# Optimization experiments

Measured on AMD Instinct MI355X. Metric: run time of the kernel, lower is better.

## Reference

```python
import jax, jax.numpy as jnp
import numpy as np

EPS = 1e-5


def _layer_norm(x, gamma, beta):
    mu = jnp.mean(x, axis=-1, keepdims=True)
    var = jnp.var(x, axis=-1, keepdims=True)
    return (x - mu) * jax.lax.rsqrt(var + EPS) * gamma + beta


def setup_inputs() -> dict:
    key = jax.random.key(0)
    B, I, H = 4096, 1024, 1024
    ks = jax.random.split(key, 6)
    x = jax.random.normal(ks[0], (B, I), dtype=jnp.float32)
    h = jax.random.normal(ks[1], (B, H), dtype=jnp.float32)
    c = jax.random.normal(ks[2], (B, H), dtype=jnp.float32)
    # nn.Linear(I+H, 4H): weight [4H, I+H], bias [4H]
    bound = 1.0 / np.sqrt(I + H)
    W = jax.random.uniform(ks[3], (4 * H, I + H), minval=-bound, maxval=bound, dtype=jnp.float32)
    b = jax.random.uniform(ks[4], (4 * H,), minval=-bound, maxval=bound, dtype=jnp.float32)
    inp = {"x": x, "h": h, "c": c, "W": W, "b": b}
    for name in ("i", "f", "g", "o", "c"):
        inp[f"ln_{name}_g"] = jnp.ones((H,), dtype=jnp.float32)
        inp[f"ln_{name}_b"] = jnp.zeros((H,), dtype=jnp.float32)
    return inp


def reference(x, h, c, W, b, ln_i_g, ln_i_b, ln_f_g, ln_f_b, ln_g_g, ln_g_b,
              ln_o_g, ln_o_b, ln_c_g, ln_c_b):
    H = h.shape[-1]
    xh = jnp.concatenate([x, h], axis=-1)              # [B, I+H]
    gates = xh @ W.T + b                               # [B, 4H]
    i_raw, f_raw, g_raw, o_raw = jnp.split(gates, 4, axis=-1)
    i = jax.nn.sigmoid(_layer_norm(i_raw, ln_i_g, ln_i_b))
    f = jax.nn.sigmoid(_layer_norm(f_raw, ln_f_g, ln_f_b))
    g = jnp.tanh(_layer_norm(g_raw, ln_g_g, ln_g_b))
    o = jax.nn.sigmoid(_layer_norm(o_raw, ln_o_g, ln_o_b))
    c_new = f * c + i * g
    h_new = o * jnp.tanh(_layer_norm(c_new, ln_c_g, ln_c_b))
    return (h_new, c_new)
```

## Files before the change

kernel.cpp:

```cpp
#include <hip/hip_runtime.h>
#include <hip/hip_bf16.h>

#define B_ROWS 4096
#define H_DIM  1024
#define K_DIM  2048
#define N_DIM  4096
#define NT     32

typedef __attribute__((ext_vector_type(8))) short bf16x8;
typedef __attribute__((ext_vector_type(4))) float f32x4;

__device__ __forceinline__ unsigned short f2bf(float f) {
  union { float f; unsigned int u; } v; v.f = f;
  unsigned int u = v.u;
  return (unsigned short)((u + 0x7fffu + ((u >> 16) & 1u)) >> 16);
}
__device__ __forceinline__ float bf2f(unsigned short u) {
  union { unsigned int u; float f; } v; v.u = ((unsigned int)u) << 16;
  return v.f;
}

__device__ __forceinline__ void gload_lds16(const void* g, void* l) {
  __builtin_amdgcn_global_load_lds(
      (const __attribute__((address_space(1))) void*)g,
      (__attribute__((address_space(3))) void*)l, 16, 0, 0);
}

__global__ __launch_bounds__(256) void pack_kernel(
    const float* __restrict__ x, const float* __restrict__ h,
    const float* __restrict__ W, unsigned short* __restrict__ Abf,
    unsigned short* __restrict__ Wbf) {
  int bid = blockIdx.x;
  if (bid < 8192) {
    int t = bid * 256 + threadIdx.x;
    int e = t * 4;
    int row = e >> 11;
    int col = e & 2047;
    const float* src = (col < 1024) ? (x + (size_t)row * 1024 + col)
                                    : (h + (size_t)row * 1024 + (col - 1024));
    float4 v = *(const float4*)src;
    ushort4 o;
    o.x = f2bf(v.x); o.y = f2bf(v.y); o.z = f2bf(v.z); o.w = f2bf(v.w);
    *(ushort4*)(Abf + e) = o;
  } else {
    int t = (bid - 8192) * 256 + threadIdx.x;
    int e = t * 4;
    float4 v = *(const float4*)(W + e);
    ushort4 o;
    o.x = f2bf(v.x); o.y = f2bf(v.y); o.z = f2bf(v.z); o.w = f2bf(v.w);
    *(ushort4*)(Wbf + e) = o;
  }
}


#define STAGE(g, kt, dst) do {                              \
    gload_lds16((g) + (size_t)(kt) * 64, (dst));            \
    gload_lds16((g) + (size_t)(kt) * 64 + 32, (dst) + 1024); } while (0)

#define WAIT_LGKM0() do {                                   \
    asm volatile("s_waitcnt lgkmcnt(0)" ::: "memory");      \
    __builtin_amdgcn_sched_barrier(0); } while (0)

#define UNR _Pragma("unroll")

#define TILE(tt, BUF, B0R, B0W)                                              \
  {                                                                          \
    char* const Lc = lds + (BUF) * 65536;                                    \
    char* const Ln = lds + ((BUF) ^ 1) * 65536;                              \
    const int kt1 = ((tt) + 1) & (NT - 1);                                   \
    const int kt2 = ((tt) + 2) & (NT - 1);                                   \
        \
    STAGE(gA1, kt1, Ln + rbA1 * 2048);                                       \
    __builtin_amdgcn_s_barrier();                                            \
    WAIT_LGKM0();                                                            \
    __builtin_amdgcn_s_setprio(1);                                           \
    UNR for (int ni = 0; ni < 2; ++ni)                                       \
      UNR for (int kk = 0; kk < 2; ++kk)                                     \
        b1[ni][kk] = *(const bf16x8*)(Lc + 32768 +                           \
            (((wn * 4 + 2 + ni) * 2 + kk) << 10) + lofs);                    \
    UNR for (int mi = 0; mi < 4; ++mi)                                       \
      UNR for (int ni = 0; ni < 2; ++ni)                                     \
        UNR for (int kk = 0; kk < 2; ++kk)                                   \
          acc[mi][ni] = __builtin_amdgcn_mfma_f32_16x16x32_bf16(             \
              a0[mi][kk], B0R[ni][kk], acc[mi][ni], 0, 0, 0);                \
    __builtin_amdgcn_s_setprio(0);                                           \
    __builtin_amdgcn_s_barrier();                                            \
         \
    STAGE(gA0, kt2, Lc + rbA0 * 2048);                                       \
    __builtin_amdgcn_s_barrier();                                            \
    WAIT_LGKM0();                                                            \
    __builtin_amdgcn_s_setprio(1);                                           \
    UNR for (int mi = 0; mi < 4; ++mi)                                       \
      UNR for (int kk = 0; kk < 2; ++kk)                                     \
        a1[mi][kk] = *(const bf16x8*)(Lc +                                   \
            (((wm * 8 + 4 + mi) * 2 + kk) << 10) + lofs);                    \
    UNR for (int mi = 0; mi < 4; ++mi)                                       \
      UNR for (int ni = 0; ni < 2; ++ni)                                     \
        UNR for (int kk = 0; kk < 2; ++kk)                                   \
          acc[mi][2 + ni] = __builtin_amdgcn_mfma_f32_16x16x32_bf16(         \
              a0[mi][kk], b1[ni][kk], acc[mi][2 + ni], 0, 0, 0);             \
    __builtin_amdgcn_s_setprio(0);                                           \
    __builtin_amdgcn_s_barrier();                                            \
                  \
    STAGE(gB0, kt2, Lc + 32768 + rbB0 * 2048);                               \
    __builtin_amdgcn_s_barrier();                                            \
    WAIT_LGKM0();                                                            \
    __builtin_amdgcn_s_setprio(1);                                           \
    UNR for (int mi = 0; mi < 4; ++mi)                                       \
      UNR for (int ni = 0; ni < 2; ++ni)                                     \
        UNR for (int kk = 0; kk < 2; ++kk)                                   \
          acc[4 + mi][2 + ni] = __builtin_amdgcn_mfma_f32_16x16x32_bf16(     \
              a1[mi][kk], b1[ni][kk], acc[4 + mi][2 + ni], 0, 0, 0);         \
    __builtin_amdgcn_s_setprio(0);                                           \
    __builtin_amdgcn_s_barrier();                                            \
          \
    STAGE(gB1, kt2, Lc + 32768 + rbB1 * 2048);                               \
    asm volatile("s_waitcnt vmcnt(6)" ::: "memory");                         \
    __builtin_amdgcn_s_barrier();                                            \
    __builtin_amdgcn_s_setprio(1);                                           \
    UNR for (int mi = 0; mi < 4; ++mi)                                       \
      UNR for (int kk = 0; kk < 2; ++kk)                                     \
        a0[mi][kk] = *(const bf16x8*)(Ln +                                   \
            (((wm * 8 + mi) * 2 + kk) << 10) + lofs);                        \
    UNR for (int ni = 0; ni < 2; ++ni)                                       \
      UNR for (int kk = 0; kk < 2; ++kk)                                     \
        B0W[ni][kk] = *(const bf16x8*)(Ln + 32768 +                          \
            (((wn * 4 + ni) * 2 + kk) << 10) + lofs);                        \
    UNR for (int mi = 0; mi < 4; ++mi)                                       \
      UNR for (int ni = 0; ni < 2; ++ni)                                     \
        UNR for (int kk = 0; kk < 2; ++kk)                                   \
          acc[4 + mi][ni] = __builtin_amdgcn_mfma_f32_16x16x32_bf16(         \
              a1[mi][kk], B0R[ni][kk], acc[4 + mi][ni], 0, 0, 0);            \
    __builtin_amdgcn_s_setprio(0);                                           \
    __builtin_amdgcn_s_barrier();                                            \
  }

__global__ __launch_bounds__(512, 2) void gemm_kernel(
    const unsigned short* __restrict__ A, const unsigned short* __restrict__ W,
    const float* __restrict__ bias, unsigned short* __restrict__ C) {
  __shared__ __align__(16) char lds[131072];

  const int tid = threadIdx.x;
  const int w = tid >> 6, l = tid & 63;
  const int wm = w >> 2, wn = w & 3;

  const int bid = blockIdx.x;
  const int xcd = bid & 7, li = bid >> 3;
  const int by = (xcd & 3) * 4 + (li >> 3);
  const int bx = ((xcd >> 2) << 3) + (li & 7);
  const int bm = by * 256, bn = bx * 256;

  const int lofs = (((l & 15) * 64) + ((l >> 4) * 16)) ^ ((l & 8) << 2);
  const int lane_r = (l >> 2) & 15;
  const int lane_c = ((l & 3) * 8) ^ (((l >> 5) & 1) * 16);

  const int rbA0 = w + (w & 4);
  const int rbA1 = rbA0 + 4;
  const int rbB0 = ((w >> 1) << 2) + (w & 1);
  const int rbB1 = rbB0 + 2;

  const unsigned short* gA0 = A + (size_t)(bm + rbA0 * 16 + lane_r) * K_DIM + lane_c;
  const unsigned short* gA1 = A + (size_t)(bm + rbA1 * 16 + lane_r) * K_DIM + lane_c;
  const unsigned short* gB0 = W + (size_t)(bn + rbB0 * 16 + lane_r) * K_DIM + lane_c;
  const unsigned short* gB1 = W + (size_t)(bn + rbB1 * 16 + lane_r) * K_DIM + lane_c;

  char* const L0 = lds;
  char* const L1 = lds + 65536;

  f32x4 acc[8][4];
#pragma unroll
  for (int i = 0; i < 8; ++i)
#pragma unroll
    for (int j = 0; j < 4; ++j) acc[i][j] = (f32x4)0.0f;

  STAGE(gA0, 0, L0 + rbA0 * 2048);
  STAGE(gA1, 0, L0 + rbA1 * 2048);
  STAGE(gB0, 0, L0 + 32768 + rbB0 * 2048);
  STAGE(gB1, 0, L0 + 32768 + rbB1 * 2048);
  STAGE(gA0, 1, L1 + rbA0 * 2048);
  STAGE(gB0, 1, L1 + 32768 + rbB0 * 2048);
  STAGE(gB1, 1, L1 + 32768 + rbB1 * 2048);
  asm volatile("s_waitcnt vmcnt(6)" ::: "memory");
  __builtin_amdgcn_s_barrier();

  bf16x8 a0[4][2], a1[4][2], b0P[2][2], b0Q[2][2], b1[2][2];

#pragma unroll
  for (int mi = 0; mi < 4; ++mi)
#pragma unroll
    for (int kk = 0; kk < 2; ++kk)
      a0[mi][kk] = *(const bf16x8*)(L0 + (((wm * 8 + mi) * 2 + kk) << 10) + lofs);
#pragma unroll
  for (int ni = 0; ni < 2; ++ni)
#pragma unroll
    for (int kk = 0; kk < 2; ++kk)
      b0P[ni][kk] = *(const bf16x8*)(L0 + 32768 + (((wn * 4 + ni) * 2 + kk) << 10) + lofs);

  for (int t = 0; t < NT; t += 2) {
    TILE(t, 0, b0P, b0Q);
    TILE(t + 1, 1, b0Q, b0P);
  }

  const int lm = l & 15, lq = l >> 4;
  float bv[4];
#pragma unroll
  for (int ni = 0; ni < 4; ++ni) bv[ni] = bias[bn + wn * 64 + ni * 16 + lm];
  unsigned short* Cb = C + (size_t)(bm + wm * 128) * N_DIM + bn + wn * 64;
#pragma unroll
  for (int mi = 0; mi < 8; ++mi)
#pragma unroll
    for (int j = 0; j < 4; ++j) {
      const size_t rofs = (size_t)(mi * 16 + lq * 4 + j) * N_DIM;
#pragma unroll
      for (int ni = 0; ni < 4; ++ni)
        Cb[rofs + ni * 16 + lm] = f2bf(acc[mi][ni][j] + bv[ni]);
    }
}

__device__ __forceinline__ float2 blk_sum2(float s, float q, float* red,
                                           int wid, int lane) {
#pragma unroll
  for (int o = 32; o >= 1; o >>= 1) {
    s += __shfl_xor(s, o, 64);
    q += __shfl_xor(q, o, 64);
  }
  __syncthreads();
  if (lane == 0) { red[wid * 2] = s; red[wid * 2 + 1] = q; }
  __syncthreads();
  s = red[0] + red[2] + red[4] + red[6];
  q = red[1] + red[3] + red[5] + red[7];
  return make_float2(s, q);
}

__device__ __forceinline__ float sigmoidf_(float x) {
  return 1.0f / (1.0f + __expf(-x));
}
__device__ __forceinline__ float tanhf_(float x) {
  return 1.0f - 2.0f / (__expf(2.0f * x) + 1.0f);
}

__global__ __launch_bounds__(256) void ln_lstm_kernel(
    const unsigned short* __restrict__ gates, const float* __restrict__ cprev,
    const float* __restrict__ g_i, const float* __restrict__ b_i,
    const float* __restrict__ g_f, const float* __restrict__ b_f,
    const float* __restrict__ g_g, const float* __restrict__ b_g,
    const float* __restrict__ g_o, const float* __restrict__ b_o,
    const float* __restrict__ g_c, const float* __restrict__ b_c,
    float* __restrict__ out) {
  const int b = blockIdx.x;
  const int t = threadIdx.x;
  const int wid = t >> 6, lane = t & 63;
  __shared__ float red[8];

  const unsigned short* grow = gates + (size_t)b * N_DIM;
  const int c0 = t * 4;

  float v[4][4];
#pragma unroll
  for (int g = 0; g < 4; g++) {
    ushort4 raw = *(const ushort4*)(grow + g * 1024 + c0);
    v[g][0] = bf2f(raw.x); v[g][1] = bf2f(raw.y);
    v[g][2] = bf2f(raw.z); v[g][3] = bf2f(raw.w);
  }

  const float4 gamma[4] = {*(const float4*)(g_i + c0), *(const float4*)(g_f + c0),
                           *(const float4*)(g_g + c0), *(const float4*)(g_o + c0)};
  const float4 beta[4]  = {*(const float4*)(b_i + c0), *(const float4*)(b_f + c0),
                           *(const float4*)(b_g + c0), *(const float4*)(b_o + c0)};

  float a[4][4];
#pragma unroll
  for (int g = 0; g < 4; g++) {
    float s = v[g][0] + v[g][1] + v[g][2] + v[g][3];
    float q = v[g][0]*v[g][0] + v[g][1]*v[g][1] + v[g][2]*v[g][2] + v[g][3]*v[g][3];
    float2 r = blk_sum2(s, q, red, wid, lane);
    float mu = r.x * (1.0f / 1024.0f);
    float var = r.y * (1.0f / 1024.0f) - mu * mu;
    float inv = rsqrtf(var + 1e-5f);
    const float* gm = (const float*)&gamma[g];
    const float* bt = (const float*)&beta[g];
#pragma unroll
    for (int j = 0; j < 4; j++) {
      float n = (v[g][j] - mu) * inv * gm[j] + bt[j];
      a[g][j] = (g == 2) ? tanhf_(n) : sigmoidf_(n);
    }
  }

  float4 cp = *(const float4*)(cprev + (size_t)b * 1024 + c0);
  const float* cpe = (const float*)&cp;
  float cn[4];
#pragma unroll
  for (int j = 0; j < 4; j++)
    cn[j] = a[1][j] * cpe[j] + a[0][j] * a[2][j];

  {
    float s = cn[0] + cn[1] + cn[2] + cn[3];
    float q = cn[0]*cn[0] + cn[1]*cn[1] + cn[2]*cn[2] + cn[3]*cn[3];
    float2 r = blk_sum2(s, q, red, wid, lane);
    float mu = r.x * (1.0f / 1024.0f);
    float var = r.y * (1.0f / 1024.0f) - mu * mu;
    float inv = rsqrtf(var + 1e-5f);
    float4 gm = *(const float4*)(g_c + c0);
    float4 bt = *(const float4*)(b_c + c0);
    const float* gme = (const float*)&gm;
    const float* bte = (const float*)&bt;
    float hn[4];
#pragma unroll
    for (int j = 0; j < 4; j++) {
      float n = (cn[j] - mu) * inv * gme[j] + bte[j];
      hn[j] = a[3][j] * tanhf_(n);
    }
    *(float4*)(out + (size_t)b * 1024 + c0) = make_float4(hn[0], hn[1], hn[2], hn[3]);
    *(float4*)(out + (size_t)B_ROWS * H_DIM + (size_t)b * 1024 + c0) =
        make_float4(cn[0], cn[1], cn[2], cn[3]);
  }
}

extern "C" void kernel_launch(void* const* d_in, const int* in_sizes, int n_in,
                              void* d_out, int out_size, void* d_ws,
                              size_t ws_size, hipStream_t stream) {
  const float* x    = (const float*)d_in[0];
  const float* h    = (const float*)d_in[1];
  const float* c    = (const float*)d_in[2];
  const float* W    = (const float*)d_in[3];
  const float* bias = (const float*)d_in[4];
  const float* ln_i_g = (const float*)d_in[5];
  const float* ln_i_b = (const float*)d_in[6];
  const float* ln_f_g = (const float*)d_in[7];
  const float* ln_f_b = (const float*)d_in[8];
  const float* ln_g_g = (const float*)d_in[9];
  const float* ln_g_b = (const float*)d_in[10];
  const float* ln_o_g = (const float*)d_in[11];
  const float* ln_o_b = (const float*)d_in[12];
  const float* ln_c_g = (const float*)d_in[13];
  const float* ln_c_b = (const float*)d_in[14];

  unsigned short* Abf = (unsigned short*)d_ws;
  unsigned short* Wbf = Abf + (size_t)B_ROWS * K_DIM;
  unsigned short* gates = Wbf + (size_t)N_DIM * K_DIM;

  pack_kernel<<<16384, 256, 0, stream>>>(x, h, W, Abf, Wbf);

  dim3 ggrid(256);
  gemm_kernel<<<ggrid, 512, 0, stream>>>(Abf, Wbf, bias, gates);

  ln_lstm_kernel<<<B_ROWS, 256, 0, stream>>>(
      gates, c, ln_i_g, ln_i_b, ln_f_g, ln_f_b, ln_g_g, ln_g_b,
      ln_o_g, ln_o_b, ln_c_g, ln_c_b, (float*)d_out);
}
```

Baseline: 102.3 us.

## Restructure GEMM main loop into four-stage K=32 pipeline with one barrier per tile

Replaces the two-buffer K=64 tile schedule, which had four barrier-separated MFMA phases per tile, with a four-buffer ring of K=32 tiles. Each tile issues one global-to-LDS prefetch three stages ahead and uses a single barrier. The LDS fragment reads for the next tile are issued before the current tile's 32 MFMAs so they can overlap. The goal is fewer barriers and a deeper prefetch to hide load latency. The cost is twice as many loop iterations with smaller per-tile work, and the loop relies on tight hand-set vmcnt and lgkmcnt counts.

```diff
diff --git a/kernel.cpp b/kernel.cpp
--- a/kernel.cpp
+++ b/kernel.cpp
@@ -5,7 +5,7 @@
 #define H_DIM  1024
 #define K_DIM  2048
 #define N_DIM  4096
-#define NT     32
+#define NT32   64
 
 typedef __attribute__((ext_vector_type(8))) short bf16x8;
 typedef __attribute__((ext_vector_type(4))) float f32x4;
@@ -53,86 +53,44 @@
 }
 
 
-#define STAGE(g, kt, dst) do {                              \
-    gload_lds16((g) + (size_t)(kt) * 64, (dst));            \
-    gload_lds16((g) + (size_t)(kt) * 64 + 32, (dst) + 1024); } while (0)
-
-#define WAIT_LGKM0() do {                                   \
-    asm volatile("s_waitcnt lgkmcnt(0)" ::: "memory");      \
-    __builtin_amdgcn_sched_barrier(0); } while (0)
-
 #define UNR _Pragma("unroll")
 
-#define TILE(tt, BUF, B0R, B0W)                                              \
+#define TILE1(tt, BUF, FRa, FRb, FWa, FWb)                                   \
   {                                                                          \
-    char* const Lc = lds + (BUF) * 65536;                                    \
-    char* const Ln = lds + ((BUF) ^ 1) * 65536;                              \
-    const int kt1 = ((tt) + 1) & (NT - 1);                                   \
-    const int kt2 = ((tt) + 2) & (NT - 1);                                   \
-        \
-    STAGE(gA1, kt1, Ln + rbA1 * 2048);                                       \
+    const int kt3 = ((tt) + 3) & (NT32 - 1);                                 \
+    char* const Ld = lds + (((BUF) + 3) & 3) * 32768;                        \
+    const unsigned short* pA = gAw + ((size_t)kt3 << 5);                     \
+    const unsigned short* pB = gBw + ((size_t)kt3 << 5);                     \
+    gload_lds16(pA, Ld + dstOfs);                                            \
+    gload_lds16(pA + 16 * K_DIM, Ld + dstOfs + 1024);                        \
+    gload_lds16(pB, Ld + 16384 + dstOfs);                                    \
+    gload_lds16(pB + 16 * K_DIM, Ld + 16384 + dstOfs + 1024);                \
+    asm volatile("s_waitcnt vmcnt(8)" ::: "memory");                         \
     __builtin_amdgcn_s_barrier();                                            \
-    WAIT_LGKM0();                                                            \
+    const char* const Ln = lds + (((BUF) + 1) & 3) * 32768;                  \
+    UNR for (int mi = 0; mi < 8; ++mi)                                       \
+      FWa[mi] = *(const bf16x8*)(Ln + (wm * 8 + mi) * 1024 + lofs);          \
+    UNR for (int ni = 0; ni < 4; ++ni)                                       \
+      FWb[ni] = *(const bf16x8*)(Ln + 16384 + (wn * 4 + ni) * 1024 + lofs);  \
+    asm volatile("s_waitcnt lgkmcnt(12)" ::: "memory");                      \
+    __builtin_amdgcn_sched_barrier(0);                                       \
     __builtin_amdgcn_s_setprio(1);                                           \
-    UNR for (int ni = 0; ni < 2; ++ni)                                       \
-      UNR for (int kk = 0; kk < 2; ++kk)                                     \
-        b1[ni][kk] = *(const bf16x8*)(Lc + 32768 +                           \
-            (((wn * 4 + 2 + ni) * 2 + kk) << 10) + lofs);                    \
-    UNR for (int mi = 0; mi < 4; ++mi)                                       \
-      UNR for (int ni = 0; ni < 2; ++ni)                                     \
-        UNR for (int kk = 0; kk < 2; ++kk)                                   \
-          acc[mi][ni] = __builtin_amdgcn_mfma_f32_16x16x32_bf16(             \
-              a0[mi][kk], B0R[ni][kk], acc[mi][ni], 0, 0, 0);                \
+    UNR for (int mi = 0; mi < 8; ++mi)                                       \
+      UNR for (int ni = 0; ni < 4; ++ni)                                     \
+        acc[mi][ni] = __builtin_amdgcn_mfma_f32_16x16x32_bf16(               \
+            FRa[mi], FRb[ni], acc[mi][ni], 0, 0, 0);                         \
     __builtin_amdgcn_s_setprio(0);                                           \
-    __builtin_amdgcn_s_barrier();                                            \
-         \
-    STAGE(gA0, kt2, Lc + rbA0 * 2048);                                       \
-    __builtin_amdgcn_s_barrier();                                            \
-    WAIT_LGKM0();                                                            \
-    __builtin_amdgcn_s_setprio(1);                                           \
-    UNR for (int mi = 0; mi < 4; ++mi)                                       \
-      UNR for (int kk = 0; kk < 2; ++kk)                                     \
-        a1[mi][kk] = *(const bf16x8*)(Lc +                                   \
-            (((wm * 8 + 4 + mi) * 2 + kk) << 10) + lofs);                    \
-    UNR for (int mi = 0; mi < 4; ++mi)                                       \
-      UNR for (int ni = 0; ni < 2; ++ni)                                     \
-        UNR for (int kk = 0; kk < 2; ++kk)                                   \
-          acc[mi][2 + ni] = __builtin_amdgcn_mfma_f32_16x16x32_bf16(         \
-              a0[mi][kk], b1[ni][kk], acc[mi][2 + ni], 0, 0, 0);             \
-    __builtin_amdgcn_s_setprio(0);                                           \
-    __builtin_amdgcn_s_barrier();                                            \
-                  \
-    STAGE(gB0, kt2, Lc + 32768 + rbB0 * 2048);                               \
-    __builtin_amdgcn_s_barrier();                                            \
-    WAIT_LGKM0();                                                            \
-    __builtin_amdgcn_s_setprio(1);                                           \
-    UNR for (int mi = 0; mi < 4; ++mi)                                       \
-      UNR for (int ni = 0; ni < 2; ++ni)                                     \
-        UNR for (int kk = 0; kk < 2; ++kk)                                   \
-          acc[4 + mi][2 + ni] = __builtin_amdgcn_mfma_f32_16x16x32_bf16(     \
-              a1[mi][kk], b1[ni][kk], acc[4 + mi][2 + ni], 0, 0, 0);         \
-    __builtin_amdgcn_s_setprio(0);                                           \
-    __builtin_amdgcn_s_barrier();                                            \
-          \
-    STAGE(gB1, kt2, Lc + 32768 + rbB1 * 2048);                               \
-    asm volatile("s_waitcnt vmcnt(6)" ::: "memory");                         \
-    __builtin_amdgcn_s_barrier();                                            \
-    __builtin_amdgcn_s_setprio(1);                                           \
-    UNR for (int mi = 0; mi < 4; ++mi)                                       \
-      UNR for (int kk = 0; kk < 2; ++kk)                                     \
-        a0[mi][kk] = *(const bf16x8*)(Ln +                                   \
-            (((wm * 8 + mi) * 2 + kk) << 10) + lofs);                        \
-    UNR for (int ni = 0; ni < 2; ++ni)                                       \
-      UNR for (int kk = 0; kk < 2; ++kk)                                     \
-        B0W[ni][kk] = *(const bf16x8*)(Ln + 32768 +                          \
-            (((wn * 4 + ni) * 2 + kk) << 10) + lofs);                        \
-    UNR for (int mi = 0; mi < 4; ++mi)                                       \
-      UNR for (int ni = 0; ni < 2; ++ni)                                     \
-        UNR for (int kk = 0; kk < 2; ++kk)                                   \
-          acc[4 + mi][ni] = __builtin_amdgcn_mfma_f32_16x16x32_bf16(         \
-              a1[mi][kk], B0R[ni][kk], acc[4 + mi][ni], 0, 0, 0);            \
-    __builtin_amdgcn_s_setprio(0);                                           \
-    __builtin_amdgcn_s_barrier();                                            \
+  }
+
+#define PSTAGE(kt, BUFOFS)                                                   \
+  {                                                                          \
+    const unsigned short* pA = gAw + ((size_t)(kt) << 5);                    \
+    const unsigned short* pB = gBw + ((size_t)(kt) << 5);                    \
+    char* const Ld = lds + (BUFOFS);                                         \
+    gload_lds16(pA, Ld + dstOfs);                                            \
+    gload_lds16(pA + 16 * K_DIM, Ld + dstOfs + 1024);                        \
+    gload_lds16(pB, Ld + 16384 + dstOfs);                                    \
+    gload_lds16(pB + 16 * K_DIM, Ld + 16384 + dstOfs + 1024);                \
   }
 
 __global__ __launch_bounds__(512, 2) void gemm_kernel(
@@ -154,18 +112,9 @@
   const int lane_r = (l >> 2) & 15;
   const int lane_c = ((l & 3) * 8) ^ (((l >> 5) & 1) * 16);
 
-  const int rbA0 = w + (w & 4);
-  const int rbA1 = rbA0 + 4;
-  const int rbB0 = ((w >> 1) << 2) + (w & 1);
-  const int rbB1 = rbB0 + 2;
-
-  const unsigned short* gA0 = A + (size_t)(bm + rbA0 * 16 + lane_r) * K_DIM + lane_c;
-  const unsigned short* gA1 = A + (size_t)(bm + rbA1 * 16 + lane_r) * K_DIM + lane_c;
-  const unsigned short* gB0 = W + (size_t)(bn + rbB0 * 16 + lane_r) * K_DIM + lane_c;
-  const unsigned short* gB1 = W + (size_t)(bn + rbB1 * 16 + lane_r) * K_DIM + lane_c;
-
-  char* const L0 = lds;
-  char* const L1 = lds + 65536;
+  const int dstOfs = w * 2048;
+  const unsigned short* gAw = A + (size_t)(bm + 32 * w + lane_r) * K_DIM + lane_c;
+  const unsigned short* gBw = W + (size_t)(bn + 32 * w + lane_r) * K_DIM + lane_c;
 
   f32x4 acc[8][4];
 #pragma unroll
@@ -173,32 +122,25 @@
 #pragma unroll
     for (int j = 0; j < 4; ++j) acc[i][j] = (f32x4)0.0f;
 
-  STAGE(gA0, 0, L0 + rbA0 * 2048);
-  STAGE(gA1, 0, L0 + rbA1 * 2048);
-  STAGE(gB0, 0, L0 + 32768 + rbB0 * 2048);
-  STAGE(gB1, 0, L0 + 32768 + rbB1 * 2048);
-  STAGE(gA0, 1, L1 + rbA0 * 2048);
-  STAGE(gB0, 1, L1 + 32768 + rbB0 * 2048);
-  STAGE(gB1, 1, L1 + 32768 + rbB1 * 2048);
-  asm volatile("s_waitcnt vmcnt(6)" ::: "memory");
+  PSTAGE(0, 0);
+  PSTAGE(1, 32768);
+  PSTAGE(2, 65536);
+  asm volatile("s_waitcnt vmcnt(8)" ::: "memory");
   __builtin_amdgcn_s_barrier();
 
-  bf16x8 a0[4][2], a1[4][2], b0P[2][2], b0Q[2][2], b1[2][2];
-
-#pragma unroll
-  for (int mi = 0; mi < 4; ++mi)
-#pragma unroll
-    for (int kk = 0; kk < 2; ++kk)
-      a0[mi][kk] = *(const bf16x8*)(L0 + (((wm * 8 + mi) * 2 + kk) << 10) + lofs);
-#pragma unroll
-  for (int ni = 0; ni < 2; ++ni)
-#pragma unroll
-    for (int kk = 0; kk < 2; ++kk)
-      b0P[ni][kk] = *(const bf16x8*)(L0 + 32768 + (((wn * 4 + ni) * 2 + kk) << 10) + lofs);
-
-  for (int t = 0; t < NT; t += 2) {
-    TILE(t, 0, b0P, b0Q);
-    TILE(t + 1, 1, b0Q, b0P);
+  bf16x8 aP[8], bP[4], aQ[8], bQ[4];
+#pragma unroll
+  for (int mi = 0; mi < 8; ++mi)
+    aP[mi] = *(const bf16x8*)(lds + (wm * 8 + mi) * 1024 + lofs);
+#pragma unroll
+  for (int ni = 0; ni < 4; ++ni)
+    bP[ni] = *(const bf16x8*)(lds + 16384 + (wn * 4 + ni) * 1024 + lofs);
+
+  for (int t = 0; t < NT32; t += 4) {
+    TILE1(t + 0, 0, aP, bP, aQ, bQ);
+    TILE1(t + 1, 1, aQ, bQ, aP, bP);
+    TILE1(t + 2, 2, aP, bP, aQ, bQ);
+    TILE1(t + 3, 3, aQ, bQ, aP, bP);
   }
 
   const int lm = l & 15, lq = l >> 4;
```

New measurement: 105.3 us. 2.9% more time.
